# Performance work log

Measured on AMD Instinct MI355X. Metric: run time of the kernel, lower is better.

Reference implementation:

```python
import jax, jax.numpy as jnp
import numpy as np

N = 25600   # total nodes
B = 256     # graphs / batch_size / LSTM seq length
F = 128     # num_feat
H = 256     # gnn_hidden
R = 512     # rnn_hidden == 2*H (forced by alm layer)
L = 2       # rnn_layers
V = 32000   # vocab
E = 409600  # edges
NPG = 100   # nodes per graph (forced by alm layer / attention reshape)


def setup_inputs() -> dict:
    key = jax.random.key(0)
    ks = jax.random.split(key, 20)
    def rn(k, shape, fan_in, scale=1.0):
        return jax.random.normal(k, shape, jnp.float32) * (scale / np.sqrt(fan_in))
    inp = {}
    inp['x'] = jax.random.normal(ks[0], (N, F), jnp.float32)
    inp['edge_index'] = jax.random.randint(ks[1], (2, E), 0, N)
    inp['bwd_edge_index'] = jnp.flip(inp['edge_index'], axis=0)
    inp['batch'] = jnp.arange(N) // NPG  # contiguous graphs, 100 nodes each
    inp['h0'] = jax.random.normal(ks[2], (L, 1, R), jnp.float32)
    inp['c0'] = jax.random.normal(ks[3], (L, 1, R), jnp.float32)
    inp['W_gnn'] = rn(ks[4], (F, H), F)
    inp['W_root'] = rn(ks[5], (H, H), H)
    inp['W_nbr'] = rn(ks[6], (H, H), H)
    inp['b_conv'] = jnp.zeros((H,), jnp.float32)
    D = 2 * H
    inp['W1'] = rn(ks[7], (D, D), D); inp['b1'] = jnp.zeros((D,), jnp.float32)
    inp['gamma'] = jnp.ones((D,), jnp.float32); inp['beta'] = jnp.zeros((D,), jnp.float32)
    inp['W2'] = rn(ks[8], (D, D), D); inp['b2'] = jnp.zeros((D,), jnp.float32)
    A = NPG * R + R  # alm input dim = rnn_hidden*100 + rnn_hidden
    inp['W_alm'] = rn(ks[9], (NPG, A), A, scale=0.1)
    inp['b_alm'] = jnp.ones((NPG,), jnp.float32)  # keeps alpha.sum() well away from 0
    inp['Wih0'] = rn(ks[10], (4 * R, D), D); inp['Whh0'] = rn(ks[11], (4 * R, R), R)
    inp['bih0'] = jnp.zeros((4 * R,), jnp.float32); inp['bhh0'] = jnp.zeros((4 * R,), jnp.float32)
    inp['Wih1'] = rn(ks[12], (4 * R, R), R); inp['Whh1'] = rn(ks[13], (4 * R, R), R)
    inp['bih1'] = jnp.zeros((4 * R,), jnp.float32); inp['bhh1'] = jnp.zeros((4 * R,), jnp.float32)
    inp['W_fc'] = rn(ks[14], (R, V), R); inp['b_fc'] = jnp.zeros((V,), jnp.float32)
    return inp


def _lstm_layer(inputs, h, c, Wih, Whh, bih, bhh):
    # inputs: (T, 1, in); carry h, c: (1, R). PyTorch gate order i, f, g, o.
    def step(carry, xt):
        h, c = carry
        g = xt @ Wih.T + bih + h @ Whh.T + bhh
        i, f, gg, o = jnp.split(g, 4, axis=-1)
        c = jax.nn.sigmoid(f) * c + jax.nn.sigmoid(i) * jnp.tanh(gg)
        h = jax.nn.sigmoid(o) * jnp.tanh(c)
        return (h, c), h
    (hT, cT), outs = jax.lax.scan(step, (h, c), inputs)
    return outs, hT, cT


def reference(x, edge_index, bwd_edge_index, batch, h0, c0, W_gnn, W_root, W_nbr, b_conv,
              W1, b1, gamma, beta, W2, b2, W_alm, b_alm,
              Wih0, Whh0, bih0, bhh0, Wih1, Whh1, bih1, bhh1, W_fc, b_fc):
    n = x.shape[0]
    x = x @ W_gnn  # (N, H)
    # GraphConv: out_i = W_root x_i + W_nbr * sum_{j->i} x_j + b.
    # (Original loops gnn_layers times from the SAME x, so only the last conv matters.)
    def conv(xx, ei):
        agg = jax.ops.segment_sum(xx[ei[0]], ei[1], num_segments=n)
        return xx @ W_root + agg @ W_nbr + b_conv
    fwd_x = jax.nn.relu(conv(x, edge_index))
    bwd_x = jax.nn.relu(conv(x, bwd_edge_index))
    xc = jnp.concatenate([fwd_x, bwd_x], axis=1)  # (N, 2H) == (N, R)
    # MLP [2H, 2H, 2H]: Lin -> BatchNorm(batch stats) -> ReLU -> (dropout off) -> Lin
    h1 = xc @ W1 + b1
    h1 = (h1 - h1.mean(0)) / jnp.sqrt(h1.var(0) + 1e-5) * gamma + beta
    x_mlp = jax.nn.relu(h1) @ W2 + b2
    # global mean pool over graphs
    counts = jax.ops.segment_sum(jnp.ones((n,), x_mlp.dtype), batch, num_segments=B)
    x_g = jax.ops.segment_sum(x_mlp, batch, num_segments=B) / counts[:, None]
    x_emb = x_g.reshape(B, 1, 2 * H)  # LSTM: seq_len=B, batch=1
    # attention over cell state (vectorized form of the nested loops):
    # alpha[l,b,:] = alm(cat(c0[l].flatten(), h3[b].flatten())); normalize by sum (NOT softmax);
    # new_c[l] = sum_b alpha[l,b,:] @ h3[b]
    h3 = xc.reshape(B, NPG, R)
    s = c0.reshape(L, R)
    Ws, Wh = W_alm[:, :R], W_alm[:, R:]
    alpha = (s @ Ws.T)[:, None, :] + (h3.reshape(B, NPG * R) @ Wh.T)[None] + b_alm  # (L,B,NPG)
    alpha = alpha / alpha.sum(-1, keepdims=True)
    new_c = jnp.einsum('lbk,bkd->ld', alpha, h3)  # (L, R)
    # 2-layer LSTM (eval mode: inter-layer dropout is identity)
    outs, hT0, cT0 = _lstm_layer(x_emb, h0[0], new_c[0:1], Wih0, Whh0, bih0, bhh0)
    outs, hT1, cT1 = _lstm_layer(outs, h0[1], new_c[1:2], Wih1, Whh1, bih1, bhh1)
    preds = (outs @ W_fc + b_fc)[:, -1, :]  # (B, V)
    return preds
```

## Files before the change

kernel.cpp:

```cpp
#include <hip/hip_runtime.h>
#include <math.h>

#define N_NODES 25600
#define F_IN    128
#define H_GNN   256
#define D_MLP   512
#define E_EDGE  409600
#define B_GR    256
#define NPG_    100
#define R_LSTM  512
#define V_OUT   32000

typedef __bf16 bf16x8 __attribute__((ext_vector_type(8)));
typedef float  f32x4  __attribute__((ext_vector_type(4)));
typedef unsigned short u16x8 __attribute__((ext_vector_type(8)));

__device__ __forceinline__ unsigned short f2bf(float x) {
    unsigned u = __builtin_bit_cast(unsigned, x);
    unsigned r = (u + 0x7FFFu + ((u >> 16) & 1u)) >> 16;
    return (unsigned short)r;
}

template<bool TRANSB>
__global__ __launch_bounds__(256)
void gemm_tile(const float* __restrict__ A, const float* __restrict__ B,
               float* __restrict__ C, const float* __restrict__ bias,
               int M, int N, int K, int lda, int ldb, int ldc, int kChunk)
{
    __shared__ float As[16][68];
    __shared__ float Bs[16][68];
    const int tid = threadIdx.x;
    const int n0 = blockIdx.x * 64;
    const int m0 = blockIdx.y * 64;
    const int z  = blockIdx.z;
    const int k0 = z * kChunk;
    const int k1 = min(K, k0 + kChunk);
    const int ty = tid >> 4, tx = tid & 15;
    float acc[4][4] = {};

    for (int kb = k0; kb < k1; kb += 16) {
        {
            const int r = tid >> 4, c = tid & 15;
            #pragma unroll
            for (int i = 0; i < 4; ++i) {
                int rr = r + i * 16;
                int gm = m0 + rr, gk = kb + c;
                As[c][rr] = (gm < M && gk < k1) ? A[gm * lda + gk] : 0.f;
            }
        }
        if (!TRANSB) {
            const int r = tid >> 6, c = tid & 63;
            #pragma unroll
            for (int i = 0; i < 4; ++i) {
                int rr = r + i * 4;
                int gk = kb + rr, gn = n0 + c;
                Bs[rr][c] = (gk < k1 && gn < N) ? B[gk * ldb + gn] : 0.f;
            }
        } else {
            const int r = tid & 15, c = tid >> 4;
            #pragma unroll
            for (int i = 0; i < 4; ++i) {
                int cc = c + i * 16;
                int gk = kb + r, gn = n0 + cc;
                Bs[r][cc] = (gk < k1 && gn < N) ? B[gn * ldb + gk] : 0.f;
            }
        }
        __syncthreads();
        #pragma unroll
        for (int kk = 0; kk < 16; ++kk) {
            float a[4], b[4];
            #pragma unroll
            for (int i = 0; i < 4; ++i) a[i] = As[kk][ty * 4 + i];
            #pragma unroll
            for (int j = 0; j < 4; ++j) b[j] = Bs[kk][tx * 4 + j];
            #pragma unroll
            for (int i = 0; i < 4; ++i)
                #pragma unroll
                for (int j = 0; j < 4; ++j)
                    acc[i][j] = fmaf(a[i], b[j], acc[i][j]);
        }
        __syncthreads();
    }

    const bool split = (gridDim.z > 1);
    #pragma unroll
    for (int i = 0; i < 4; ++i) {
        int gm = m0 + ty * 4 + i;
        if (gm >= M) continue;
        #pragma unroll
        for (int j = 0; j < 4; ++j) {
            int gn = n0 + tx * 4 + j;
            if (gn >= N) continue;
            float v = acc[i][j];
            if (bias != nullptr && z == 0) v += bias[gn];
            if (split) atomicAdd(&C[gm * ldc + gn], v);
            else       C[gm * ldc + gn] = v;
        }
    }
}

__global__ __launch_bounds__(256)
void mfma_gemm(const unsigned short* __restrict__ A,
               const unsigned short* __restrict__ Bt,
               float* __restrict__ C, const float* __restrict__ bias,
               int M, int N, int K, int lda, int ldb, int ldc, int kChunk)
{
    __shared__ unsigned short As[128][40];
    __shared__ unsigned short Bs[128][40];
    const int tid  = threadIdx.x;
    const int lane = tid & 63;
    const int wv   = tid >> 6;
    const int wr   = wv >> 1, wc = wv & 1;
    const int n0 = blockIdx.x * 128;
    const int m0 = blockIdx.y * 128;
    const int z  = blockIdx.z;
    const int k0 = z * kChunk;
    const int k1 = min(K, k0 + kChunk);

    const int srow = tid >> 2;
    const int skoff = (tid & 3) * 8;

    f32x4 acc[4][4] = {};

    for (int kb = k0; kb < k1; kb += 32) {
        #pragma unroll
        for (int p = 0; p < 2; ++p) {
            int row = p * 64 + srow;
            u16x8 va = *(const u16x8*)(A + (long)(m0 + row) * lda + kb + skoff);
            *(u16x8*)&As[row][skoff] = va;
            int gb = n0 + row;
            u16x8 vb = {0, 0, 0, 0, 0, 0, 0, 0};
            if (gb < N) vb = *(const u16x8*)(Bt + (long)gb * ldb + kb + skoff);
            *(u16x8*)&Bs[row][skoff] = vb;
        }
        __syncthreads();
        bf16x8 af[4], bfr[4];
        #pragma unroll
        for (int fm = 0; fm < 4; ++fm)
            af[fm] = *(const bf16x8*)&As[wr * 64 + fm * 16 + (lane & 15)][(lane >> 4) * 8];
        #pragma unroll
        for (int fn = 0; fn < 4; ++fn)
            bfr[fn] = *(const bf16x8*)&Bs[wc * 64 + fn * 16 + (lane & 15)][(lane >> 4) * 8];
        #pragma unroll
        for (int fm = 0; fm < 4; ++fm)
            #pragma unroll
            for (int fn = 0; fn < 4; ++fn)
                acc[fm][fn] = __builtin_amdgcn_mfma_f32_16x16x32_bf16(
                    af[fm], bfr[fn], acc[fm][fn], 0, 0, 0);
        __syncthreads();
    }

    const bool split = (gridDim.z > 1);
    #pragma unroll
    for (int fm = 0; fm < 4; ++fm) {
        int row = m0 + wr * 64 + fm * 16 + ((lane >> 4) << 2);
        #pragma unroll
        for (int fn = 0; fn < 4; ++fn) {
            int col = n0 + wc * 64 + fn * 16 + (lane & 15);
            if (col >= N) continue;
            f32x4 v = acc[fm][fn];
            #pragma unroll
            for (int r = 0; r < 4; ++r) {
                float o = v[r];
                if (bias != nullptr && z == 0) o += bias[col];
                if (split) atomicAdd(&C[(long)(row + r) * ldc + col], o);
                else       C[(long)(row + r) * ldc + col] = o;
            }
        }
    }
}

__global__ void castbf(const float* __restrict__ in, unsigned short* __restrict__ out,
                       long n) {
    long stride = (long)gridDim.x * blockDim.x * 4;
    for (long j = ((long)blockIdx.x * blockDim.x + threadIdx.x) * 4; j < n; j += stride) {
        float4 v = *(const float4*)(in + j);
        ushort4 o;
        o.x = f2bf(v.x); o.y = f2bf(v.y); o.z = f2bf(v.z); o.w = f2bf(v.w);
        *(ushort4*)(out + j) = o;
    }
}
__global__ void cast_strided(const float* __restrict__ in, unsigned short* __restrict__ out,
                             int cols, long ldin, long off) {
    const int r = blockIdx.y;
    int c = (blockIdx.x * blockDim.x + threadIdx.x) * 4;
    if (c < cols) {
        float4 v = *(const float4*)(in + (long)r * ldin + off + c);
        ushort4 o;
        o.x = f2bf(v.x); o.y = f2bf(v.y); o.z = f2bf(v.z); o.w = f2bf(v.w);
        *(ushort4*)(out + (long)r * cols + c) = o;
    }
}
__global__ __launch_bounds__(256)
void transcast(const float* __restrict__ in, unsigned short* __restrict__ out,
               int R, int C) {
    __shared__ unsigned short t[64][72];
    const int c0 = blockIdx.x * 64, r0 = blockIdx.y * 64;
    const int tid = threadIdx.x;
    const int rr = tid >> 2, cg = (tid & 3) * 16;
    #pragma unroll
    for (int i = 0; i < 4; ++i) {
        float4 v = *(const float4*)(in + (long)(r0 + rr) * C + c0 + cg + i * 4);
        t[cg + i * 4 + 0][rr] = f2bf(v.x);
        t[cg + i * 4 + 1][rr] = f2bf(v.y);
        t[cg + i * 4 + 2][rr] = f2bf(v.z);
        t[cg + i * 4 + 3][rr] = f2bf(v.w);
    }
    __syncthreads();
    const int cc = tid >> 2, kg = (tid & 3) * 16;
    #pragma unroll
    for (int i = 0; i < 2; ++i) {
        u16x8 v = *(const u16x8*)&t[cc][kg + i * 8];
        *(u16x8*)(out + (long)(c0 + cc) * R + r0 + kg + i * 8) = v;
    }
}

__global__ void zero_f32(float* p, long n) {
    for (long i = (long)blockIdx.x * blockDim.x + threadIdx.x; i < n;
         i += (long)gridDim.x * blockDim.x) p[i] = 0.f;
}
__global__ void zero_i32(int* p, long n) {
    for (long i = (long)blockIdx.x * blockDim.x + threadIdx.x; i < n;
         i += (long)gridDim.x * blockDim.x) p[i] = 0;
}
__global__ void addvec_kernel(const float* a, const float* b, float* o, int n) {
    int i = blockIdx.x * blockDim.x + threadIdx.x;
    if (i < n) o[i] = a[i] + b[i];
}

__global__ void hist_kernel(const int* __restrict__ key, int* counts, int E) {
    int i = blockIdx.x * blockDim.x + threadIdx.x;
    if (i < E) atomicAdd(&counts[key[i]], 1);
}
__global__ __launch_bounds__(256)
void scan_kernel(const int* __restrict__ counts, int* rowptr, int* cursor, int n) {
    __shared__ int buf[256];
    __shared__ int carry_s;
    const int tid = threadIdx.x;
    if (tid == 0) carry_s = 0;
    __syncthreads();
    const int nch = (n + 255) / 256;
    for (int ch = 0; ch < nch; ++ch) {
        int i = ch * 256 + tid;
        int v = (i < n) ? counts[i] : 0;
        buf[tid] = v;
        __syncthreads();
        for (int off = 1; off < 256; off <<= 1) {
            int add = (tid >= off) ? buf[tid - off] : 0;
            __syncthreads();
            buf[tid] += add;
            __syncthreads();
        }
        int incl = buf[tid];
        int base = carry_s;
        if (i < n) {
            rowptr[i + 1] = base + incl;
            cursor[i]     = base + incl - v;
        }
        if (ch == 0 && tid == 0) rowptr[0] = 0;
        __syncthreads();
        if (tid == 255) carry_s = base + incl;
        __syncthreads();
    }
}
__global__ void scatter_kernel(const int* __restrict__ key, const int* __restrict__ val,
                               int* cursor, int* sorted, int E) {
    int i = blockIdx.x * blockDim.x + threadIdx.x;
    if (i < E) {
        int pos = atomicAdd(&cursor[key[i]], 1);
        sorted[pos] = val[i];
    }
}
__global__ __launch_bounds__(256)
void agg_conv_kernel(const float* __restrict__ xr, const float* __restrict__ xn,
                     const int* __restrict__ rowptr, const int* __restrict__ sorted,
                     float* __restrict__ xc, int halfOff) {
    const int n = blockIdx.x, tid = threadIdx.x;
    float acc = xr[n * H_GNN + tid];
    const int s = rowptr[n], e = rowptr[n + 1];
    for (int t = s; t < e; ++t) {
        int src = sorted[t];
        acc += xn[src * H_GNN + tid];
    }
    xc[n * D_MLP + halfOff + tid] = fmaxf(acc, 0.f);
}

__global__ __launch_bounds__(512)
void colstat_kernel(const float* __restrict__ h1, float* colsum, float* colsq) {
    const int c = threadIdx.x;
    const int r0 = blockIdx.x * 128;
    float s = 0.f, s2 = 0.f;
    for (int r = 0; r < 128; ++r) {
        float v = h1[(r0 + r) * D_MLP + c];
        s += v; s2 += v * v;
    }
    atomicAdd(&colsum[c], s);
    atomicAdd(&colsq[c], s2);
}
__global__ void finalize_stats(const float* colsum, const float* colsq,
                               const float* gamma, const float* beta,
                               float* scalev, float* shiftv) {
    int c = threadIdx.x;
    float m  = colsum[c] * (1.f / N_NODES);
    float vr = colsq[c] * (1.f / N_NODES) - m * m;
    float g  = gamma[c] * rsqrtf(vr + 1e-5f);
    scalev[c] = g;
    shiftv[c] = beta[c] - m * g;
}
__global__ void norm_relu(float* h, const float* __restrict__ sc,
                          const float* __restrict__ sh, long n) {
    for (long i = (long)blockIdx.x * blockDim.x + threadIdx.x; i < n;
         i += (long)gridDim.x * blockDim.x) {
        int c = (int)(i & 511);
        h[i] = fmaxf(fmaf(h[i], sc[c], sh[c]), 0.f);
    }
}
__global__ __launch_bounds__(512)
void pool_kernel(const float* __restrict__ hrelu, float* P) {
    const int b = blockIdx.x, c = threadIdx.x;
    float s = 0.f;
    for (int i = 0; i < NPG_; ++i) s += hrelu[(b * NPG_ + i) * D_MLP + c];
    P[b * D_MLP + c] = s * (1.f / NPG_);
}
__global__ void sw_kernel(const float* __restrict__ c0, const float* __restrict__ W_alm,
                          float* sW) {
    int i = blockIdx.x * blockDim.x + threadIdx.x;
    if (i < 2 * NPG_) {
        int l = i / NPG_, p = i % NPG_;
        float s = 0.f;
        for (int k = 0; k < R_LSTM; ++k) s += c0[l * R_LSTM + k] * W_alm[p * 51712 + k];
        sW[l * NPG_ + p] = s;
    }
}
__global__ __launch_bounds__(128)
void alpha_kernel(const float* __restrict__ sW, const float* __restrict__ hW,
                  const float* __restrict__ b_alm, float* __restrict__ alpha) {
    const int lb = blockIdx.x;
    const int l = lb >> 8, b = lb & 255;
    const int p = threadIdx.x;
    __shared__ float red[128];
    float v = 0.f;
    if (p < NPG_) v = sW[l * NPG_ + p] + hW[b * NPG_ + p] + b_alm[p];
    red[p] = v;
    __syncthreads();
    for (int s = 64; s > 0; s >>= 1) {
        if (p < s) red[p] += red[p + s];
        __syncthreads();
    }
    float inv = 1.f / red[0];
    if (p < NPG_) alpha[lb * NPG_ + p] = v * inv;
}
__global__ __launch_bounds__(512)
void newc_kernel(const float* __restrict__ alpha, const float* __restrict__ xc,
                 float* new_c) {
    const int l = blockIdx.y, chunk = blockIdx.x, c = threadIdx.x;
    const int r0 = chunk * 800;
    float acc = 0.f;
    for (int r = r0; r < r0 + 800; ++r)
        acc += alpha[l * N_NODES + r] * xc[r * D_MLP + c];
    atomicAdd(&new_c[l * D_MLP + c], acc);
}

#define CANARY 0x7FC00000u
#define SPIN_MAX 20000

__device__ __forceinline__ unsigned coh_load_u(const unsigned* p) {
    return __hip_atomic_load(p, __ATOMIC_RELAXED, __HIP_MEMORY_SCOPE_AGENT);
}
__device__ __forceinline__ void coh_store_f(float* p, float v) {
    __hip_atomic_store(p, v, __ATOMIC_RELAXED, __HIP_MEMORY_SCOPE_AGENT);
}

__global__ void lstm_init_kernel(const float* __restrict__ h0,
                                 float* h0buf, float* h1buf) {
    int i = blockIdx.x * blockDim.x + threadIdx.x;
    if (i < 512) { h0buf[i] = h0[i]; h1buf[i] = h0[512 + i]; }
    for (int j = 512 + i; j < 257 * 512; j += gridDim.x * blockDim.x) {
        ((unsigned*)h0buf)[j] = CANARY;
        ((unsigned*)h1buf)[j] = CANARY;
    }
}

__global__ __launch_bounds__(512)
void lstm_kernel(const float* __restrict__ inp0, const float* __restrict__ Whh0,
                 const float* __restrict__ Wih1, const float* __restrict__ Whh1,
                 const float* __restrict__ b1s, const float* __restrict__ new_c,
                 float* h0buf, float* h1buf)
{
    const int tid  = threadIdx.x;
    const int lane = tid & 63;
    const int w    = tid >> 6;
    const int blk  = blockIdx.x;
    const int layer = blk >> 5;
    const int base  = (blk & 31) * 16;
    const int gate  = lane >> 4;
    const int hid   = lane & 15;
    const int rowg  = gate * 512 + base + hid;

    __shared__ float partial[2][8][64];

    if (layer == 0) {
        float wr[64];
        {
            const float4* wp = (const float4*)(Whh0 + (long)rowg * 512 + w * 64);
            #pragma unroll
            for (int i = 0; i < 16; ++i) {
                float4 v = wp[i];
                wr[4*i] = v.x; wr[4*i+1] = v.y; wr[4*i+2] = v.z; wr[4*i+3] = v.w;
            }
        }
        float c = (w == 0 && lane < 16) ? new_c[base + lane] : 0.f;
        const unsigned* src_u = (const unsigned*)h0buf + w * 64 + lane;
        for (int t = 0; t < 256; ++t) {
            float ipv = (w == 0) ? inp0[t * 2048 + rowg] : 0.f;
            unsigned hu; int guard = 0;
            for (;;) {
                hu = coh_load_u(src_u + t * 512);
                if (!__any(hu == CANARY)) break;
                if (++guard > SPIN_MAX) break;
                if (guard > 32) __builtin_amdgcn_s_sleep(1);
            }
            float hv = __uint_as_float(hu);
            float acc = 0.f;
            #pragma unroll
            for (int j = 0; j < 64; ++j)
                acc = fmaf(wr[j], __shfl(hv, j), acc);
            partial[t & 1][w][lane] = acc;
            __syncthreads();
            if (w == 0) {
                float g = ipv;
                #pragma unroll
                for (int ww = 0; ww < 8; ++ww) g += partial[t & 1][ww][lane];
                float a = (gate == 2) ? tanhf(g) : 1.f / (1.f + expf(-g));
                float fv = __shfl(a, lane + 16);
                float gv = __shfl(a, lane + 32);
                float ov = __shfl(a, lane + 48);
                if (lane < 16) {
                    c = fv * c + a * gv;
                    float h = ov * tanhf(c);
                    coh_store_f(h0buf + (t + 1) * 512 + base + lane, h);
                }
            }
        }
    } else {
        const float* Wsel = (w < 4) ? Wih1 : Whh1;
        const int koff = (w & 3) * 128;
        float wrA[64], wrB[64];
        {
            const float4* wp = (const float4*)(Wsel + (long)rowg * 512 + koff);
            #pragma unroll
            for (int i = 0; i < 16; ++i) {
                float4 v = wp[i];
                wrA[4*i] = v.x; wrA[4*i+1] = v.y; wrA[4*i+2] = v.z; wrA[4*i+3] = v.w;
            }
            #pragma unroll
            for (int i = 0; i < 16; ++i) {
                float4 v = wp[16 + i];
                wrB[4*i] = v.x; wrB[4*i+1] = v.y; wrB[4*i+2] = v.z; wrB[4*i+3] = v.w;
            }
        }
        float bsum = (w == 0) ? b1s[rowg] : 0.f;
        float c = (w == 0 && lane < 16) ? new_c[512 + base + lane] : 0.f;
        for (int t = 0; t < 256; ++t) {
            const unsigned* xsrc = (w < 4)
                ? (const unsigned*)h0buf + (t + 1) * 512 + koff
                : (const unsigned*)h1buf + t * 512 + koff;
            unsigned hu0, hu1; int guard = 0;
            for (;;) {
                hu0 = coh_load_u(xsrc + lane);
                hu1 = coh_load_u(xsrc + 64 + lane);
                if (!__any((hu0 == CANARY) || (hu1 == CANARY))) break;
                if (++guard > SPIN_MAX) break;
                if (guard > 32) __builtin_amdgcn_s_sleep(1);
            }
            float hv0 = __uint_as_float(hu0), hv1 = __uint_as_float(hu1);
            float acc = 0.f;
            #pragma unroll
            for (int j = 0; j < 64; ++j)
                acc = fmaf(wrA[j], __shfl(hv0, j), acc);
            #pragma unroll
            for (int j = 0; j < 64; ++j)
                acc = fmaf(wrB[j], __shfl(hv1, j), acc);
            partial[t & 1][w][lane] = acc;
            __syncthreads();
            if (w == 0) {
                float g = bsum;
                #pragma unroll
                for (int ww = 0; ww < 8; ++ww) g += partial[t & 1][ww][lane];
                float a = (gate == 2) ? tanhf(g) : 1.f / (1.f + expf(-g));
                float fv = __shfl(a, lane + 16);
                float gv = __shfl(a, lane + 32);
                float ov = __shfl(a, lane + 48);
                if (lane < 16) {
                    c = fv * c + a * gv;
                    float h = ov * tanhf(c);
                    coh_store_f(h1buf + (t + 1) * 512 + base + lane, h);
                }
            }
        }
    }
}

extern "C" void kernel_launch(void* const* d_in, const int* in_sizes, int n_in,
                              void* d_out, int out_size, void* d_ws, size_t ws_size,
                              hipStream_t stream)
{
    const float* x      = (const float*)d_in[0];
    const int*   ei     = (const int*)d_in[1];
    const float* h0     = (const float*)d_in[4];
    const float* c0     = (const float*)d_in[5];
    const float* W_gnn  = (const float*)d_in[6];
    const float* W_root = (const float*)d_in[7];
    const float* W_nbr  = (const float*)d_in[8];
    const float* b_conv = (const float*)d_in[9];
    const float* W1     = (const float*)d_in[10];
    const float* b1     = (const float*)d_in[11];
    const float* gamma  = (const float*)d_in[12];
    const float* beta   = (const float*)d_in[13];
    const float* W2     = (const float*)d_in[14];
    const float* b2     = (const float*)d_in[15];
    const float* W_alm  = (const float*)d_in[16];
    const float* b_alm  = (const float*)d_in[17];
    const float* Wih0   = (const float*)d_in[18];
    const float* Whh0   = (const float*)d_in[19];
    const float* bih0   = (const float*)d_in[20];
    const float* bhh0   = (const float*)d_in[21];
    const float* Wih1   = (const float*)d_in[22];
    const float* Whh1   = (const float*)d_in[23];
    const float* bih1   = (const float*)d_in[24];
    const float* bhh1   = (const float*)d_in[25];
    const float* W_fc   = (const float*)d_in[26];
    const float* b_fc   = (const float*)d_in[27];
    float* out = (float*)d_out;
    float* ws  = (float*)d_ws;

    const int* ei0 = ei;
    const int* ei1 = ei + E_EDGE;

    float* xr = ws;
    float* xn = ws + 6553600L;
    float* xc = ws + 13107200L;
    float* h1m = ws;
    unsigned short* Wfct  = (unsigned short*)ws;
    unsigned short* Walmb = (unsigned short*)(ws + 8500000L);
    unsigned short* ob    = (unsigned short*)(ws + 11200000L);
    long o = 26214400L;
    float* Wgr   = ws + o; o += 32768;
    float* Wgn   = ws + o; o += 32768;
    int*   counts= (int*)(ws + o); o += 25600;
    int*   rowptr= (int*)(ws + o); o += 25601;
    int*   cursor= (int*)(ws + o); o += 25600;
    int*   sorted= (int*)(ws + o); o += 409600;
    float* colsum= ws + o; o += 512;
    float* colsq = ws + o; o += 512;
    float* scalev= ws + o; o += 512;
    float* shiftv= ws + o; o += 512;
    float* P     = ws + o; o += 131072;
    float* x_g   = ws + o; o += 131072;
    float* hW    = ws + o; o += 25600;
    float* sW    = ws + o; o += 200;
    float* alphav= ws + o; o += 51200;
    float* newc  = ws + o; o += 1024;
    float* b0s   = ws + o; o += 2048;
    float* b1s   = ws + o; o += 2048;
    float* inp0  = ws + o; o += 524288;
    float* h0st  = ws + o; o += 131584;
    float* h1st  = ws + o; o += 131584;
    unsigned short* xcb = (unsigned short*)(ws + o); o += 3276800;

    gemm_tile<false><<<dim3(4, 2, 1), 256, 0, stream>>>(W_gnn, W_root, Wgr, nullptr,
        128, 256, 256, 256, 256, 256, 256);
    gemm_tile<false><<<dim3(4, 2, 1), 256, 0, stream>>>(W_gnn, W_nbr, Wgn, nullptr,
        128, 256, 256, 256, 256, 256, 256);
    gemm_tile<false><<<dim3(4, 400, 1), 256, 0, stream>>>(x, Wgr, xr, b_conv,
        N_NODES, 256, 128, 128, 256, 256, 128);
    gemm_tile<false><<<dim3(4, 400, 1), 256, 0, stream>>>(x, Wgn, xn, nullptr,
        N_NODES, 256, 128, 128, 256, 256, 128);
    zero_i32<<<dim3(100), 256, 0, stream>>>(counts, 25600);
    hist_kernel<<<dim3(1600), 256, 0, stream>>>(ei1, counts, E_EDGE);
    scan_kernel<<<dim3(1), 256, 0, stream>>>(counts, rowptr, cursor, 25600);
    scatter_kernel<<<dim3(1600), 256, 0, stream>>>(ei1, ei0, cursor, sorted, E_EDGE);
    agg_conv_kernel<<<dim3(25600), 256, 0, stream>>>(xr, xn, rowptr, sorted, xc, 0);
    zero_i32<<<dim3(100), 256, 0, stream>>>(counts, 25600);
    hist_kernel<<<dim3(1600), 256, 0, stream>>>(ei0, counts, E_EDGE);
    scan_kernel<<<dim3(1), 256, 0, stream>>>(counts, rowptr, cursor, 25600);
    scatter_kernel<<<dim3(1600), 256, 0, stream>>>(ei0, ei1, cursor, sorted, E_EDGE);
    agg_conv_kernel<<<dim3(25600), 256, 0, stream>>>(xr, xn, rowptr, sorted, xc, 256);
    gemm_tile<false><<<dim3(8, 400, 1), 256, 0, stream>>>(xc, W1, h1m, b1,
        N_NODES, 512, 512, 512, 512, 512, 512);
    zero_f32<<<dim3(4), 256, 0, stream>>>(colsum, 1024);
    colstat_kernel<<<dim3(200), 512, 0, stream>>>(h1m, colsum, colsq);
    finalize_stats<<<dim3(1), 512, 0, stream>>>(colsum, colsq, gamma, beta, scalev, shiftv);
    norm_relu<<<dim3(2048), 256, 0, stream>>>(h1m, scalev, shiftv, (long)N_NODES * 512);
    pool_kernel<<<dim3(256), 512, 0, stream>>>(h1m, P);
    gemm_tile<false><<<dim3(8, 4, 1), 256, 0, stream>>>(P, W2, x_g, b2,
        256, 512, 512, 512, 512, 512, 512);
    transcast<<<dim3(500, 8), 256, 0, stream>>>(W_fc, Wfct, 512, V_OUT);
    cast_strided<<<dim3(50, 100), 256, 0, stream>>>(W_alm, Walmb, 51200, 51712L, 512L);
    castbf<<<dim3(1024), 256, 0, stream>>>(xc, xcb, 13107200L);
    zero_f32<<<dim3(25), 256, 0, stream>>>(hW, 25600);
    mfma_gemm<<<dim3(1, 2, 32), 256, 0, stream>>>(xcb, Walmb, hW, nullptr,
        256, 100, 51200, 51200, 51200, 100, 1600);
    sw_kernel<<<dim3(1), 256, 0, stream>>>(c0, W_alm, sW);
    alpha_kernel<<<dim3(512), 128, 0, stream>>>(sW, hW, b_alm, alphav);
    zero_f32<<<dim3(1), 256, 0, stream>>>(newc, 1024);
    newc_kernel<<<dim3(32, 2), 512, 0, stream>>>(alphav, xc, newc);
    addvec_kernel<<<dim3(8), 256, 0, stream>>>(bih0, bhh0, b0s, 2048);
    addvec_kernel<<<dim3(8), 256, 0, stream>>>(bih1, bhh1, b1s, 2048);
    gemm_tile<true><<<dim3(32, 4, 1), 256, 0, stream>>>(x_g, Wih0, inp0, b0s,
        256, 2048, 512, 512, 512, 2048, 512);
    lstm_init_kernel<<<dim3(64), 512, 0, stream>>>(h0, h0st, h1st);
    lstm_kernel<<<dim3(64), 512, 0, stream>>>(inp0, Whh0, Wih1, Whh1, b1s, newc,
                                              h0st, h1st);
    castbf<<<dim3(128), 256, 0, stream>>>(h1st + 512, ob, 131072L);
    mfma_gemm<<<dim3(250, 2, 1), 256, 0, stream>>>(ob, Wfct, out, b_fc,
        256, V_OUT, 512, 512, 512, V_OUT, 512);
}
```

Before: 2.206 ms.

## Add 128x128 FP32 GEMM, fuse root/neighbor projections, parallelize CSR scan

Adds a 128x128-tile FP32 GEMM with 8x8 register blocking per thread and uses it for both the fused node projection and the 25600x512x512 MLP GEMM. The root and neighbor weight products are concatenated into one 128x512 matrix, so a single GEMM produces both halves and the aggregation kernel reads one interleaved buffer. The single-block serial prefix scan is replaced with a three-kernel chunked scan (per-chunk scan, scan of chunk totals, fixup) to remove a long serial launch. Workspace offsets are reorganised and 64-bit indexing is added, which means more register pressure in the GEMM and a different memory layout to keep consistent.

```diff
diff --git a/kernel.cpp b/kernel.cpp
--- a/kernel.cpp
+++ b/kernel.cpp
@@ -95,6 +95,62 @@
             if (bias != nullptr && z == 0) v += bias[gn];
             if (split) atomicAdd(&C[gm * ldc + gn], v);
             else       C[gm * ldc + gn] = v;
+        }
+    }
+}
+
+__global__ __launch_bounds__(256)
+void gemm_f32_big(const float* __restrict__ A, const float* __restrict__ B,
+                  float* __restrict__ C, const float* __restrict__ bias,
+                  int M, int N, int K, int lda, int ldb, int ldc)
+{
+    __shared__ float As[8][128];
+    __shared__ float Bs[8][128];
+    const int tid = threadIdx.x;
+    const int tx = tid & 15, ty = tid >> 4;
+    const int n0 = blockIdx.x * 128, m0 = blockIdx.y * 128;
+    float acc[8][8] = {};
+
+    for (int kb = 0; kb < K; kb += 8) {
+        {
+            int r = tid >> 1, c = (tid & 1) * 4;
+            float4 v = *(const float4*)(A + (long)(m0 + r) * lda + kb + c);
+            As[c + 0][r] = v.x; As[c + 1][r] = v.y;
+            As[c + 2][r] = v.z; As[c + 3][r] = v.w;
+        }
+        {
+            int r = tid >> 5, c = (tid & 31) * 4;
+            *(float4*)&Bs[r][c] = *(const float4*)(B + (long)(kb + r) * ldb + n0 + c);
+        }
+        __syncthreads();
+        #pragma unroll
+        for (int kk = 0; kk < 8; ++kk) {
+            float a[8], b[8];
+            *(float4*)&a[0] = *(const float4*)&As[kk][ty * 8];
+            *(float4*)&a[4] = *(const float4*)&As[kk][ty * 8 + 4];
+            *(float4*)&b[0] = *(const float4*)&Bs[kk][tx * 8];
+            *(float4*)&b[4] = *(const float4*)&Bs[kk][tx * 8 + 4];
+            #pragma unroll
+            for (int i = 0; i < 8; ++i)
+                #pragma unroll
+                for (int j = 0; j < 8; ++j)
+                    acc[i][j] = fmaf(a[i], b[j], acc[i][j]);
+        }
+        __syncthreads();
+    }
+
+    #pragma unroll
+    for (int i = 0; i < 8; ++i) {
+        int gm = m0 + ty * 8 + i;
+        #pragma unroll
+        for (int j = 0; j < 8; j += 4) {
+            int gn = n0 + tx * 8 + j;
+            float4 v = {acc[i][j], acc[i][j+1], acc[i][j+2], acc[i][j+3]};
+            if (bias != nullptr) {
+                v.x += bias[gn]; v.y += bias[gn + 1];
+                v.z += bias[gn + 2]; v.w += bias[gn + 3];
+            }
+            *(float4*)(C + (long)gm * ldc + gn) = v;
         }
     }
 }
@@ -227,40 +283,56 @@
     int i = blockIdx.x * blockDim.x + threadIdx.x;
     if (i < n) o[i] = a[i] + b[i];
 }
+__global__ void concat_bias(const float* __restrict__ b_conv, float* bc2) {
+    int i = blockIdx.x * blockDim.x + threadIdx.x;
+    if (i < 512) bc2[i] = (i < 256) ? b_conv[i] : 0.f;
+}
 
 __global__ void hist_kernel(const int* __restrict__ key, int* counts, int E) {
     int i = blockIdx.x * blockDim.x + threadIdx.x;
     if (i < E) atomicAdd(&counts[key[i]], 1);
 }
 __global__ __launch_bounds__(256)
-void scan_kernel(const int* __restrict__ counts, int* rowptr, int* cursor, int n) {
+void scan_chunk(const int* __restrict__ counts, int* __restrict__ rowptr,
+                int* __restrict__ tops, int n) {
     __shared__ int buf[256];
-    __shared__ int carry_s;
     const int tid = threadIdx.x;
-    if (tid == 0) carry_s = 0;
+    int i = blockIdx.x * 256 + tid;
+    int v = (i < n) ? counts[i] : 0;
+    buf[tid] = v;
     __syncthreads();
-    const int nch = (n + 255) / 256;
-    for (int ch = 0; ch < nch; ++ch) {
-        int i = ch * 256 + tid;
-        int v = (i < n) ? counts[i] : 0;
-        buf[tid] = v;
-        __syncthreads();
-        for (int off = 1; off < 256; off <<= 1) {
-            int add = (tid >= off) ? buf[tid - off] : 0;
-            __syncthreads();
-            buf[tid] += add;
-            __syncthreads();
-        }
-        int incl = buf[tid];
-        int base = carry_s;
-        if (i < n) {
-            rowptr[i + 1] = base + incl;
-            cursor[i]     = base + incl - v;
-        }
-        if (ch == 0 && tid == 0) rowptr[0] = 0;
-        __syncthreads();
-        if (tid == 255) carry_s = base + incl;
-        __syncthreads();
+    for (int off = 1; off < 256; off <<= 1) {
+        int add = (tid >= off) ? buf[tid - off] : 0;
+        __syncthreads();
+        buf[tid] += add;
+        __syncthreads();
+    }
+    if (i < n) rowptr[i + 1] = buf[tid];
+    if (tid == 255) tops[blockIdx.x] = buf[255];
+}
+__global__ __launch_bounds__(128)
+void scan_tops(int* tops, int nt) {
+    __shared__ int b[128];
+    int tid = threadIdx.x;
+    int v = (tid < nt) ? tops[tid] : 0;
+    b[tid] = v;
+    __syncthreads();
+    for (int off = 1; off < 128; off <<= 1) {
+        int add = (tid >= off) ? b[tid - off] : 0;
+        __syncthreads();
+        b[tid] += add;
+        __syncthreads();
+    }
+    if (tid < nt) tops[tid] = b[tid] - v;
+}
+__global__ void scan_fixup(const int* __restrict__ counts, int* __restrict__ rowptr,
+                           int* __restrict__ cursor, const int* __restrict__ tops, int n) {
+    int i = blockIdx.x * blockDim.x + threadIdx.x;
+    if (i < n) {
+        int r = rowptr[i + 1] + tops[i >> 8];
+        rowptr[i + 1] = r;
+        cursor[i] = r - counts[i];
+        if (i == 0) rowptr[0] = 0;
     }
 }
 __global__ void scatter_kernel(const int* __restrict__ key, const int* __restrict__ val,
@@ -272,17 +344,15 @@
     }
 }
 __global__ __launch_bounds__(256)
-void agg_conv_kernel(const float* __restrict__ xr, const float* __restrict__ xn,
+void agg_conv_kernel(const float* __restrict__ xrn,
                      const int* __restrict__ rowptr, const int* __restrict__ sorted,
-                     float* __restrict__ xc, int halfOff) {
+                     float* __restrict__ xc, int outOff) {
     const int n = blockIdx.x, tid = threadIdx.x;
-    float acc = xr[n * H_GNN + tid];
+    float acc = xrn[(long)n * 512 + tid];
     const int s = rowptr[n], e = rowptr[n + 1];
-    for (int t = s; t < e; ++t) {
-        int src = sorted[t];
-        acc += xn[src * H_GNN + tid];
-    }
-    xc[n * D_MLP + halfOff + tid] = fmaxf(acc, 0.f);
+    for (int t = s; t < e; ++t)
+        acc += xrn[(long)sorted[t] * 512 + 256 + tid];
+    xc[(long)n * 512 + outOff + tid] = fmaxf(acc, 0.f);
 }
 
 __global__ __launch_bounds__(512)
@@ -291,7 +361,7 @@
     const int r0 = blockIdx.x * 128;
     float s = 0.f, s2 = 0.f;
     for (int r = 0; r < 128; ++r) {
-        float v = h1[(r0 + r) * D_MLP + c];
+        float v = h1[(long)(r0 + r) * D_MLP + c];
         s += v; s2 += v * v;
     }
     atomicAdd(&colsum[c], s);
@@ -319,7 +389,7 @@
 void pool_kernel(const float* __restrict__ hrelu, float* P) {
     const int b = blockIdx.x, c = threadIdx.x;
     float s = 0.f;
-    for (int i = 0; i < NPG_; ++i) s += hrelu[(b * NPG_ + i) * D_MLP + c];
+    for (int i = 0; i < NPG_; ++i) s += hrelu[(long)(b * NPG_ + i) * D_MLP + c];
     P[b * D_MLP + c] = s * (1.f / NPG_);
 }
 __global__ void sw_kernel(const float* __restrict__ c0, const float* __restrict__ W_alm,
@@ -357,7 +427,7 @@
     const int r0 = chunk * 800;
     float acc = 0.f;
     for (int r = r0; r < r0 + 800; ++r)
-        acc += alpha[l * N_NODES + r] * xc[r * D_MLP + c];
+        acc += alpha[l * N_NODES + r] * xc[(long)r * D_MLP + c];
     atomicAdd(&new_c[l * D_MLP + c], acc);
 }
 
@@ -537,20 +607,19 @@
     const int* ei0 = ei;
     const int* ei1 = ei + E_EDGE;
 
-    float* xr = ws;
-    float* xn = ws + 6553600L;
-    float* xc = ws + 13107200L;
+    float* xrn = ws;
     float* h1m = ws;
     unsigned short* Wfct  = (unsigned short*)ws;
     unsigned short* Walmb = (unsigned short*)(ws + 8500000L);
     unsigned short* ob    = (unsigned short*)(ws + 11200000L);
+    float* xc = ws + 13107200L;
     long o = 26214400L;
-    float* Wgr   = ws + o; o += 32768;
-    float* Wgn   = ws + o; o += 32768;
+    float* Wc    = ws + o; o += 65536;
     int*   counts= (int*)(ws + o); o += 25600;
     int*   rowptr= (int*)(ws + o); o += 25601;
     int*   cursor= (int*)(ws + o); o += 25600;
     int*   sorted= (int*)(ws + o); o += 409600;
+    int*   tops  = (int*)(ws + o); o += 128;
     float* colsum= ws + o; o += 512;
     float* colsq = ws + o; o += 512;
     float* scalev= ws + o; o += 512;
@@ -563,31 +632,36 @@
     float* newc  = ws + o; o += 1024;
     float* b0s   = ws + o; o += 2048;
     float* b1s   = ws + o; o += 2048;
-    float* inp0  = ws + o; o += 524288;
-    float* h0st  = ws + o; o += 131584;
-    float* h1st  = ws + o; o += 131584;
-    unsigned short* xcb = (unsigned short*)(ws + o); o += 3276800;
-
-    gemm_tile<false><<<dim3(4, 2, 1), 256, 0, stream>>>(W_gnn, W_root, Wgr, nullptr,
-        128, 256, 256, 256, 256, 256, 256);
-    gemm_tile<false><<<dim3(4, 2, 1), 256, 0, stream>>>(W_gnn, W_nbr, Wgn, nullptr,
-        128, 256, 256, 256, 256, 256, 256);
-    gemm_tile<false><<<dim3(4, 400, 1), 256, 0, stream>>>(x, Wgr, xr, b_conv,
-        N_NODES, 256, 128, 128, 256, 256, 128);
-    gemm_tile<false><<<dim3(4, 400, 1), 256, 0, stream>>>(x, Wgn, xn, nullptr,
-        N_NODES, 256, 128, 128, 256, 256, 128);
+    float* bc2   = ws + o; o += 512;
+    unsigned short* xcb = (unsigned short*)(ws + o);
+    float* inp0  = ws + o;
+    float* h0st  = ws + o + 524288;
+    float* h1st  = ws + o + 655872;
+    o += 6553600;
+
+    gemm_tile<false><<<dim3(4, 2, 1), 256, 0, stream>>>(W_gnn, W_root, Wc, nullptr,
+        128, 256, 256, 256, 256, 512, 256);
+    gemm_tile<false><<<dim3(4, 2, 1), 256, 0, stream>>>(W_gnn, W_nbr, Wc + 256, nullptr,
+        128, 256, 256, 256, 256, 512, 256);
+    concat_bias<<<dim3(2), 256, 0, stream>>>(b_conv, bc2);
+    gemm_f32_big<<<dim3(4, 200), 256, 0, stream>>>(x, Wc, xrn, bc2,
+        N_NODES, 512, 128, 128, 512, 512);
     zero_i32<<<dim3(100), 256, 0, stream>>>(counts, 25600);
     hist_kernel<<<dim3(1600), 256, 0, stream>>>(ei1, counts, E_EDGE);
-    scan_kernel<<<dim3(1), 256, 0, stream>>>(counts, rowptr, cursor, 25600);
+    scan_chunk<<<dim3(100), 256, 0, stream>>>(counts, rowptr, tops, 25600);
+    scan_tops<<<dim3(1), 128, 0, stream>>>(tops, 100);
+    scan_fixup<<<dim3(100), 256, 0, stream>>>(counts, rowptr, cursor, tops, 25600);
     scatter_kernel<<<dim3(1600), 256, 0, stream>>>(ei1, ei0, cursor, sorted, E_EDGE);
-    agg_conv_kernel<<<dim3(25600), 256, 0, stream>>>(xr, xn, rowptr, sorted, xc, 0);
+    agg_conv_kernel<<<dim3(25600), 256, 0, stream>>>(xrn, rowptr, sorted, xc, 0);
     zero_i32<<<dim3(100), 256, 0, stream>>>(counts, 25600);
     hist_kernel<<<dim3(1600), 256, 0, stream>>>(ei0, counts, E_EDGE);
-    scan_kernel<<<dim3(1), 256, 0, stream>>>(counts, rowptr, cursor, 25600);
+    scan_chunk<<<dim3(100), 256, 0, stream>>>(counts, rowptr, tops, 25600);
+    scan_tops<<<dim3(1), 128, 0, stream>>>(tops, 100);
+    scan_fixup<<<dim3(100), 256, 0, stream>>>(counts, rowptr, cursor, tops, 25600);
     scatter_kernel<<<dim3(1600), 256, 0, stream>>>(ei0, ei1, cursor, sorted, E_EDGE);
-    agg_conv_kernel<<<dim3(25600), 256, 0, stream>>>(xr, xn, rowptr, sorted, xc, 256);
-    gemm_tile<false><<<dim3(8, 400, 1), 256, 0, stream>>>(xc, W1, h1m, b1,
-        N_NODES, 512, 512, 512, 512, 512, 512);
+    agg_conv_kernel<<<dim3(25600), 256, 0, stream>>>(xrn, rowptr, sorted, xc, 256);
+    gemm_f32_big<<<dim3(4, 200), 256, 0, stream>>>(xc, W1, h1m, b1,
+        N_NODES, 512, 512, 512, 512, 512);
     zero_f32<<<dim3(4), 256, 0, stream>>>(colsum, 1024);
     colstat_kernel<<<dim3(200), 512, 0, stream>>>(h1m, colsum, colsq);
     finalize_stats<<<dim3(1), 512, 0, stream>>>(colsum, colsq, gamma, beta, scalev, shiftv);
```

After: 1.868 ms. -15.3%, faster.
